# Optimization experiments

Measured on AMD Instinct MI355X. Metric: run time of the kernel, lower is better.

Reference implementation:

```python
import jax, jax.numpy as jnp
import numpy as np

Q = 9          # D2Q9
G = 8          # dihedral group of the square
X = YD = 768   # spatial grid
HID = 32       # tau_net hidden width
N_IN = 6       # moments with order <= 2 (indices 0..5, contiguous by construction)
LOWER_TAU = 0.8


def _build_stencil():
    # D2Q9 velocities and weights
    e = np.array([[0, 0], [1, 0], [0, 1], [-1, 0], [0, -1],
                  [1, 1], [-1, 1], [-1, -1], [1, -1]], dtype=np.float64)
    w = np.array([4 / 9] + [1 / 9] * 4 + [1 / 36] * 4, dtype=np.float64)
    # natural moment matrix: rows are monomials ex^px * ey^py, ordered so that
    # moment_order = [0,1,1,2,2,2,3,3,4]  ->  in_indices=[0..5], out_indices=[6,7,8]
    exps = [(0, 0), (1, 0), (0, 1), (2, 0), (1, 1), (0, 2), (2, 1), (1, 2), (2, 2)]
    M = np.stack([e[:, 0] ** px * e[:, 1] ** py for px, py in exps])  # [Q, Q]
    Minv = np.linalg.inv(M)
    # symmetry group of the square: 4 rotations x {id, x-axis reflection}
    rots = [np.array([[np.cos(a), -np.sin(a)], [np.sin(a), np.cos(a)]])
            for a in (0.0, np.pi / 2, np.pi, 3 * np.pi / 2)]
    refl = np.array([[1.0, 0.0], [0.0, -1.0]])
    Rs = rots + [r @ refl for r in rots]
    perms = []
    for R in Rs:
        Re = np.rint(e @ R.T)
        P = np.zeros((Q, Q))
        for i in range(Q):
            j = int(np.where((e == Re[i]).all(axis=1))[0][0])
            P[j, i] = 1.0  # velocity i maps to velocity j under R
        perms.append(P)
    P = np.stack(perms)                                   # [G, Q, Q]
    actions = np.einsum('qp,gpr,rs->gqs', M, P, Minv)      # moment action  M P M^-1
    Pt = P.transpose(0, 2, 1)                              # P^-1 = P^T
    inv_actions = np.einsum('qp,gpr,rs->gqs', M, Pt, Minv)
    return (M.astype(np.float32), Minv.astype(np.float32),
            actions.astype(np.float32), inv_actions.astype(np.float32),
            e.astype(np.float32), w.astype(np.float32))


def setup_inputs() -> dict:
    key = jax.random.key(0)
    kf, k1, k2, k3 = jax.random.split(key, 4)
    M, Minv, actions, inv_actions, e, w = _build_stencil()
    f = jax.random.uniform(kf, (Q, X, YD), dtype=jnp.float32)
    s = 0.1
    return {
        'f': f,
        'M': jnp.asarray(M), 'Minv': jnp.asarray(Minv),
        'actions': jnp.asarray(actions), 'inv_actions': jnp.asarray(inv_actions),
        'e': jnp.asarray(e), 'w': jnp.asarray(w),
        'W1': jax.random.normal(k1, (N_IN, HID), jnp.float32) * s,
        'b1': jnp.zeros((HID,), jnp.float32),
        'W2': jax.random.normal(k2, (HID, HID), jnp.float32) * s,
        'b2': jnp.zeros((HID,), jnp.float32),
        'W3': jax.random.normal(k3, (HID, Q - N_IN), jnp.float32) * s,
        'b3': jnp.zeros((Q - N_IN,), jnp.float32),
    }


def reference(f, M, Minv, actions, inv_actions, e, w, W1, b1, W2, b2, W3, b3):
    # --- moment transform: m = M f, moved to channel-last [X, Y, Q] ---
    m = jnp.einsum('qp,pxy->xyq', M, f)
    # --- equivariant tau net on low-order moments ---
    x_in = m[..., :N_IN]                                   # in_indices = 0..5
    Ainv = inv_actions[:, :N_IN, :N_IN]                    # [G, 6, 6]
    A = actions[:, N_IN:, N_IN:]                           # [G, 3, 3] (out_indices)
    xg = jnp.einsum('gij,xyj->gxyi', Ainv, x_in)           # [G, X, Y, 6]
    h = jax.nn.relu(xg @ W1 + b1)
    h = jax.nn.relu(h @ W2 + b2)
    o = h @ W3 + b3                                        # [G, X, Y, 3]
    out = jnp.einsum('gij,gxyj->xyi', A, o)                # sum over group -> [X, Y, 3]
    tau_hi = 1.5 + jax.nn.elu(out)                         # gt_half: > 0.5
    taus = jnp.full(m.shape, LOWER_TAU, m.dtype).at[..., N_IN:].set(tau_hi)
    # --- equilibrium moments: meq = M feq(rho, u) (quadratic BGK, cs^2=1/3) ---
    rho = m[..., 0:1]                                      # natural moments: m0=rho
    u = m[..., 1:3] / rho                                  # m1,m2 = momentum
    eu = jnp.einsum('qd,xyd->xyq', e, u)
    usq = jnp.sum(u * u, axis=-1, keepdims=True)
    feq = w * rho * (1.0 + 3.0 * eu + 4.5 * eu * eu - 1.5 * usq)
    meq = jnp.einsum('qp,xyp->xyq', M, feq)
    # --- MRT collision + inverse transform ---
    m_post = m - (m - meq) / taus
    return jnp.einsum('pq,xyq->pxy', Minv, m_post)
```

## Files before the change

kernel.cpp:

```cpp
#include <hip/hip_runtime.h>
#include <hip/hip_bf16.h>
#include <math.h>

#define Q 9
#define NPIX (768 * 768)

typedef short bf16x8 __attribute__((ext_vector_type(8)));
typedef short s16x2 __attribute__((ext_vector_type(2)));
typedef float f32x4 __attribute__((ext_vector_type(4)));
typedef float f32x16 __attribute__((ext_vector_type(16)));
typedef int i32x4 __attribute__((ext_vector_type(4)));

#define A3LOV 512
#define A3HIV 1024
#define A2LOV 1536
#define A2HIV 1600
#define B3TF  6656
#define WSHORTS 13312
#define WVEC4   (WSHORTS / 8)

__device__ __forceinline__ int hidmap(int k) {
    return (k & 3) + 8 * ((k >> 2) & 1) + 4 * (k >> 3);
}

__device__ __forceinline__ unsigned short f2bf(float x) {
    unsigned u = __builtin_bit_cast(unsigned, x);
    unsigned r = u + 0x7FFFu + ((u >> 16) & 1u);
    return (unsigned short)(r >> 16);
}

__device__ __forceinline__ unsigned pk2(float e, float o) {
    __hip_bfloat162 h = __float22bfloat162_rn(make_float2(e, o));
    unsigned u;
    __builtin_memcpy(&u, &h, 4);
    return u;
}

__device__ __forceinline__ unsigned relu2(unsigned d) {
    s16x2 v = __builtin_bit_cast(s16x2, d);
    const s16x2 z = {0, 0};
    v = __builtin_elementwise_max(v, z);
    return __builtin_bit_cast(unsigned, v);
}

__device__ __forceinline__ bf16x8 mk8(unsigned w0, unsigned w1, unsigned w2, unsigned w3) {
    i32x4 t = {(int)w0, (int)w1, (int)w2, (int)w3};
    return __builtin_bit_cast(bf16x8, t);
}

__global__ void prep_kernel(const float* __restrict__ actions,
                            const float* __restrict__ inv_actions,
                            const float* __restrict__ W1,
                            const float* __restrict__ b1,
                            const float* __restrict__ W2,
                            const float* __restrict__ W3,
                            const float* __restrict__ b3,
                            short* __restrict__ wsb,
                            float* __restrict__ wsf) {
    const int idx = blockIdx.x * 256 + threadIdx.x;
    if (idx < 4096) {
        int j = idx & 7, l = (idx >> 3) & 63, g = idx >> 9;
        int m = l & 31, k = (l >> 5) * 8 + j;
        float v = 0.f;
        if (k < 6) {
            #pragma unroll
            for (int i = 0; i < 6; i++)
                v += inv_actions[g * 81 + i * 9 + k] * W1[i * 32 + m];
        } else if (k == 6) v = b1[m];
        wsb[idx] = (short)f2bf(v);
    } else if (idx < 8192) {
        int t = idx - 4096;
        int j = t & 7, l = (t >> 3) & 63, g = t >> 9;
        int m = l & 31, kk = (l >> 5) * 8 + j, h = hidmap(kk);
        float v = 0.f;
        if (m < 3) {
            #pragma unroll
            for (int j3 = 0; j3 < 3; j3++)
                v += W3[h * 3 + j3] * actions[g * 81 + (6 + m) * 9 + (6 + j3)];
        }
        wsb[idx] = (short)f2bf(v);
    } else if (idx < 12288) {
        int t = idx - 8192;
        int j = t & 7, l = (t >> 3) & 63, g = t >> 9;
        int m = l & 31, kk = (l >> 5) * 8 + j, h = 16 + hidmap(kk);
        float v = 0.f;
        if (m < 3) {
            #pragma unroll
            for (int j3 = 0; j3 < 3; j3++)
                v += W3[h * 3 + j3] * actions[g * 81 + (6 + m) * 9 + (6 + j3)];
        }
        wsb[idx] = (short)f2bf(v);
    } else if (idx < 12800) {
        int t = idx - 12288;
        int j = t & 7, l = (t >> 3) & 63;
        int m = l & 31, kk = (l >> 5) * 8 + j;
        wsb[idx] = (short)f2bf(W2[hidmap(kk) * 32 + m]);
    } else if (idx < 13312) {
        int t = idx - 12800;
        int j = t & 7, l = (t >> 3) & 63;
        int m = l & 31, kk = (l >> 5) * 8 + j;
        wsb[idx] = (short)f2bf(W2[(16 + hidmap(kk)) * 32 + m]);
    } else if (idx < 13315) {
        int t = idx - 13312;
        float acc = 0.f;
        for (int g = 0; g < 8; g++)
            #pragma unroll
            for (int j = 0; j < 3; j++)
                acc += actions[g * 81 + (6 + t) * 9 + (6 + j)] * b3[j];
        wsf[B3TF + t] = acc;
    }
}

#define MLP_BODY(WA1, W3LO, W3HI, B1F, OACC)                                          \
    {                                                                                 \
        f32x16 C1 = __builtin_amdgcn_mfma_f32_32x32x16_bf16(WA1, B1F, z16, 0, 0, 0);  \
        bf16x8 B2lo = mk8(relu2(pk2(C1[0], C1[1])), relu2(pk2(C1[2], C1[3])),         \
                          relu2(pk2(C1[4], C1[5])), relu2(pk2(C1[6], C1[7])));        \
        bf16x8 B2hi = mk8(relu2(pk2(C1[8], C1[9])), relu2(pk2(C1[10], C1[11])),       \
                          relu2(pk2(C1[12], C1[13])), relu2(pk2(C1[14], C1[15])));    \
        f32x16 C2 = __builtin_amdgcn_mfma_f32_32x32x16_bf16(a2hi, B2hi, c2i, 0, 0, 0);\
        C2 = __builtin_amdgcn_mfma_f32_32x32x16_bf16(a2lo, B2lo, C2, 0, 0, 0);        \
        bf16x8 B3lo = mk8(relu2(pk2(C2[0], C2[1])), relu2(pk2(C2[2], C2[3])),         \
                          relu2(pk2(C2[4], C2[5])), relu2(pk2(C2[6], C2[7])));        \
        bf16x8 B3hi = mk8(relu2(pk2(C2[8], C2[9])), relu2(pk2(C2[10], C2[11])),       \
                          relu2(pk2(C2[12], C2[13])), relu2(pk2(C2[14], C2[15])));    \
        OACC = __builtin_amdgcn_mfma_f32_32x32x16_bf16(W3HI, B3hi, OACC, 0, 0, 0);    \
        OACC = __builtin_amdgcn_mfma_f32_32x32x16_bf16(W3LO, B3lo, OACC, 0, 0, 0);    \
    }

#define MOMENTS_PK(F0,F1,F2,F3,F4,F5,F6,F7,F8, MP0, MP1, MP2)                         \
    {                                                                                 \
        float sa = F5 + F6, sb = F7 + F8, sc = F5 - F6, sd = F7 - F8;                 \
        float sab = sa + sb;                                                          \
        float m4_ = sc + sd;                                                          \
        float p13 = F1 + F3, d13 = F1 - F3, p24 = F2 + F4, d24 = F2 - F4;             \
        float m0_ = F0 + p13 + p24 + sab;                                             \
        float m1_ = d13 + (sc - sd);                                                  \
        float m2_ = d24 + (sa - sb);                                                  \
        float m3_ = p13 + sab;                                                        \
        float m5_ = p24 + sab;                                                        \
        MP0 = pk2(m0_, m1_); MP1 = pk2(m2_, m3_); MP2 = pk2(m4_, m5_);                \
    }

__device__ __forceinline__ void epilogue(float fr0, float fr1, float fr2, float fr3,
                                         float fr4, float fr5, float fr6, float fr7,
                                         float fr8, f32x4 ov, int p,
                                         float* __restrict__ out) {
    float tinv[3];
    #pragma unroll
    for (int i = 0; i < 3; i++) {
        float o = ov[i];
        float el = (o > 0.f) ? o : (__expf(o) - 1.f);
        tinv[i] = __builtin_amdgcn_rcpf(1.5f + el);
    }
    float sa = fr5 + fr6, sb = fr7 + fr8, sc = fr5 - fr6, sd = fr7 - fr8;
    float p13 = fr1 + fr3, p24 = fr2 + fr4;
    float rho = fr0 + p13 + p24 + (sa + sb);
    float m1 = (fr1 - fr3) + (sc - sd);
    float m2 = (fr2 - fr4) + (sa - sb);

    float ir = __builtin_amdgcn_rcpf(rho);
    float ux = m1 * ir, uy = m2 * ir;
    float usq = ux * ux + uy * uy;
    float base = 1.f - 1.5f * usq;
    float w1r = rho * (1.f / 9.f), w5r = rho * (1.f / 36.f);
    float bx = 3.f * ux, ax = fmaf(4.5f * ux, ux, base);
    float feq1 = w1r * (ax + bx), feq3 = w1r * (ax - bx);
    float by = 3.f * uy, ay = fmaf(4.5f * uy, uy, base);
    float feq2 = w1r * (ay + by), feq4 = w1r * (ay - by);
    float ss = ux + uy, bs = 3.f * ss, as_ = fmaf(4.5f * ss, ss, base);
    float feq5 = w5r * (as_ + bs), feq7 = w5r * (as_ - bs);
    float dd = uy - ux, bd = 3.f * dd, ad = fmaf(4.5f * dd, dd, base);
    float feq6 = w5r * (ad + bd), feq8 = w5r * (ad - bd);

    float g1 = fr1 - feq1, g2 = fr2 - feq2, g3 = fr3 - feq3, g4 = fr4 - feq4;
    float g5 = fr5 - feq5, g6 = fr6 - feq6, g7 = fr7 - feq7, g8 = fr8 - feq8;
    float pa = g1 + g3, pb = g2 + g4;
    float ea = g5 + g6, eb = g7 + g8, ec = g5 - g6, ed = g7 - g8;
    float eab = ea + eb;
    float m3p = pa + eab, m5p = pb + eab, m8p = eab;
    float m6p = ea - eb, m4p = ec + ed, m7p = ec - ed;

    float d3 = 1.25f * m3p, h3 = 0.625f * m3p;
    float d5 = 1.25f * m5p, h5 = 0.625f * m5p;
    float k4 = 0.3125f * m4p;
    float h6 = (0.5f * tinv[0]) * m6p, k6 = 0.5f * h6;
    float h7 = (0.5f * tinv[1]) * m7p, k7 = 0.5f * h7;
    float d8 = tinv[2] * m8p, h8 = 0.5f * d8, k8 = 0.5f * h8;

    float c0 = d8 - d3 - d5;
    float c1 = h3 - h7 - h8;
    float c2 = h5 - h6 - h8;
    float c3 = h3 + h7 - h8;
    float c4 = h5 + h6 - h8;
    float sA = k4 + k7, sB = k6 + k8, sC = k4 + k8;
    float sD = k6 + k7, sE = k7 + k8, sF = k4 + k6;
    float c5 = sA + sB, c6 = sB - sA, c7 = sC - sD, c8 = sE - sF;

    __builtin_nontemporal_store(fr0 - c0, &out[0 * NPIX + p]);
    __builtin_nontemporal_store(fr1 - c1, &out[1 * NPIX + p]);
    __builtin_nontemporal_store(fr2 - c2, &out[2 * NPIX + p]);
    __builtin_nontemporal_store(fr3 - c3, &out[3 * NPIX + p]);
    __builtin_nontemporal_store(fr4 - c4, &out[4 * NPIX + p]);
    __builtin_nontemporal_store(fr5 - c5, &out[5 * NPIX + p]);
    __builtin_nontemporal_store(fr6 - c6, &out[6 * NPIX + p]);
    __builtin_nontemporal_store(fr7 - c7, &out[7 * NPIX + p]);
    __builtin_nontemporal_store(fr8 - c8, &out[8 * NPIX + p]);
}

__global__ __launch_bounds__(256, 3) void lbm_kernel(
    const float* __restrict__ f,
    const float* __restrict__ Minv,
    const float* __restrict__ w,
    const float* __restrict__ b2,
    const short* __restrict__ wsb,
    const float* __restrict__ wsf,
    float* __restrict__ out) {
    __shared__ float oL[4][64][4];
    __shared__ __align__(16) short wlds[WSHORTS];
    (void)Minv;
    (void)w;

    const int tid = threadIdx.x;
    const int wv = tid >> 6;
    const int l = tid & 63;
    const int hi = l >> 5;

    {
        const i32x4* src = (const i32x4*)wsb;
        i32x4* dst = (i32x4*)wlds;
        for (int i = tid; i < WVEC4; i += 256) dst[i] = src[i];
    }

    float b30 = wsf[B3TF + 0], b31 = wsf[B3TF + 1], b32 = wsf[B3TF + 2];
    f32x16 c2i;
    #pragma unroll
    for (int r = 0; r < 16; r++) {
        const int base = (r & 3) + 8 * (r >> 2);
        c2i[r] = hi ? b2[base + 4] : b2[base];
    }
    f32x16 oinit;
    #pragma unroll
    for (int r = 0; r < 16; r++) oinit[r] = 0.f;
    oinit[0] = hi ? 0.f : b30;
    oinit[1] = hi ? 0.f : b31;
    oinit[2] = hi ? 0.f : b32;
    f32x16 z16;
    #pragma unroll
    for (int r = 0; r < 16; r++) z16[r] = 0.f;

    __syncthreads();
    const bf16x8* wl = (const bf16x8*)wlds;
    bf16x8 a2lo = wl[A2LOV + l], a2hi = wl[A2HIV + l];

    const unsigned CONE = 0x00003F80u;
    const int s0 = (l & 31) << 2;
    const int s1 = s0 | (32 << 2);
    const int pbase = blockIdx.x * 768;

    #pragma unroll 1
    for (int t = 0; t < 3; t++) {
        const int p = pbase + t * 256 + tid;

        unsigned mp0, mp1, mp2;
        {
            float a0 = f[0 * NPIX + p], a1 = f[1 * NPIX + p], a2 = f[2 * NPIX + p];
            float a3 = f[3 * NPIX + p], a4 = f[4 * NPIX + p], a5 = f[5 * NPIX + p];
            float a6 = f[6 * NPIX + p], a7 = f[7 * NPIX + p], a8 = f[8 * NPIX + p];
            MOMENTS_PK(a0, a1, a2, a3, a4, a5, a6, a7, a8, mp0, mp1, mp2);
        }

        bf16x8 B1A = mk8((unsigned)__builtin_amdgcn_ds_bpermute(s0, (int)mp0),
                         (unsigned)__builtin_amdgcn_ds_bpermute(s0, (int)mp1),
                         (unsigned)__builtin_amdgcn_ds_bpermute(s0, (int)mp2), CONE);
        bf16x8 B1B = mk8((unsigned)__builtin_amdgcn_ds_bpermute(s1, (int)mp0),
                         (unsigned)__builtin_amdgcn_ds_bpermute(s1, (int)mp1),
                         (unsigned)__builtin_amdgcn_ds_bpermute(s1, (int)mp2), CONE);

        f32x16 oaccA = oinit, oaccB = oinit;

        bf16x8 wa1 = wl[l], w3lo = wl[A3LOV + l], w3hi = wl[A3HIV + l];
        #pragma unroll 1
        for (int g = 0; g < 7; g++) {
            const int gn = g + 1;
            bf16x8 na1  = wl[gn * 64 + l];
            bf16x8 n3lo = wl[A3LOV + gn * 64 + l];
            bf16x8 n3hi = wl[A3HIV + gn * 64 + l];
            MLP_BODY(wa1, w3lo, w3hi, B1A, oaccA);
            MLP_BODY(wa1, w3lo, w3hi, B1B, oaccB);
            wa1 = na1; w3lo = n3lo; w3hi = n3hi;
        }
        int p2 = p;
        asm("" : "+v"(p2));
        float r0 = f[0 * NPIX + p2], r1 = f[1 * NPIX + p2], r2 = f[2 * NPIX + p2];
        float r3 = f[3 * NPIX + p2], r4 = f[4 * NPIX + p2], r5 = f[5 * NPIX + p2];
        float r6 = f[6 * NPIX + p2], r7 = f[7 * NPIX + p2], r8 = f[8 * NPIX + p2];
        MLP_BODY(wa1, w3lo, w3hi, B1A, oaccA);
        MLP_BODY(wa1, w3lo, w3hi, B1B, oaccB);

        if (hi == 0) {
            const int lc = l & 31;
            f32x4 t0 = {oaccA[0], oaccA[1], oaccA[2], oaccA[3]};
            *(f32x4*)&oL[wv][lc][0] = t0;
            f32x4 t1 = {oaccB[0], oaccB[1], oaccB[2], oaccB[3]};
            *(f32x4*)&oL[wv][32 + lc][0] = t1;
        }
        f32x4 ov = *(const f32x4*)&oL[wv][l][0];

        epilogue(r0, r1, r2, r3, r4, r5, r6, r7, r8, ov, p, out);
    }
}

extern "C" void kernel_launch(void* const* d_in, const int* in_sizes, int n_in,
                              void* d_out, int out_size, void* d_ws, size_t ws_size,
                              hipStream_t stream) {
    const float* f           = (const float*)d_in[0];
    const float* Minv        = (const float*)d_in[2];
    const float* actions     = (const float*)d_in[3];
    const float* inv_actions = (const float*)d_in[4];
    const float* w           = (const float*)d_in[6];
    const float* W1          = (const float*)d_in[7];
    const float* b1          = (const float*)d_in[8];
    const float* W2          = (const float*)d_in[9];
    const float* b2          = (const float*)d_in[10];
    const float* W3          = (const float*)d_in[11];
    const float* b3          = (const float*)d_in[12];
    float* outp = (float*)d_out;
    short* wsb = (short*)d_ws;
    float* wsf = (float*)d_ws;

    prep_kernel<<<53, 256, 0, stream>>>(actions, inv_actions, W1, b1, W2, W3, b3, wsb, wsf);
    lbm_kernel<<<NPIX / 768, 256, 0, stream>>>(f, Minv, w, b2, wsb, wsf, outp);
}
```

Baseline: 121.1 us.

## Process one tile per block and shrink MLP output accumulators to scalars

Each block now handles 256 pixels instead of looping over three tiles, so the grid grows threefold and launch bounds rise to 4 blocks per CU. The layer-3 MFMA now accumulates into a fresh zeroed tile each group, and only three scalar values are summed into registers instead of keeping two 16-wide accumulators live. The b3 bias is added in the epilogue. This is meant to lower register pressure and raise occupancy, at the cost of reloading the weight table into LDS three times as often and issuing extra adds.

After: 121.2 us. About the same (+0.0%).

```diff
diff --git a/kernel.cpp b/kernel.cpp
--- a/kernel.cpp
+++ b/kernel.cpp
@@ -111,7 +111,7 @@
     }
 }
 
-#define MLP_BODY(WA1, W3LO, W3HI, B1F, OACC)                                          \
+#define MLP_BODY(WA1, W3LO, W3HI, B1F, A0, A1, A2)                                    \
     {                                                                                 \
         f32x16 C1 = __builtin_amdgcn_mfma_f32_32x32x16_bf16(WA1, B1F, z16, 0, 0, 0);  \
         bf16x8 B2lo = mk8(relu2(pk2(C1[0], C1[1])), relu2(pk2(C1[2], C1[3])),         \
@@ -124,8 +124,9 @@
                           relu2(pk2(C2[4], C2[5])), relu2(pk2(C2[6], C2[7])));        \
         bf16x8 B3hi = mk8(relu2(pk2(C2[8], C2[9])), relu2(pk2(C2[10], C2[11])),       \
                           relu2(pk2(C2[12], C2[13])), relu2(pk2(C2[14], C2[15])));    \
-        OACC = __builtin_amdgcn_mfma_f32_32x32x16_bf16(W3HI, B3hi, OACC, 0, 0, 0);    \
-        OACC = __builtin_amdgcn_mfma_f32_32x32x16_bf16(W3LO, B3lo, OACC, 0, 0, 0);    \
+        f32x16 C3 = __builtin_amdgcn_mfma_f32_32x32x16_bf16(W3HI, B3hi, z16, 0, 0, 0);\
+        C3 = __builtin_amdgcn_mfma_f32_32x32x16_bf16(W3LO, B3lo, C3, 0, 0, 0);        \
+        A0 += C3[0]; A1 += C3[1]; A2 += C3[2];                                        \
     }
 
 #define MOMENTS_PK(F0,F1,F2,F3,F4,F5,F6,F7,F8, MP0, MP1, MP2)                         \
@@ -142,22 +143,111 @@
         MP0 = pk2(m0_, m1_); MP1 = pk2(m2_, m3_); MP2 = pk2(m4_, m5_);                \
     }
 
-__device__ __forceinline__ void epilogue(float fr0, float fr1, float fr2, float fr3,
-                                         float fr4, float fr5, float fr6, float fr7,
-                                         float fr8, f32x4 ov, int p,
-                                         float* __restrict__ out) {
+__global__ __launch_bounds__(256, 4) void lbm_kernel(
+    const float* __restrict__ f,
+    const float* __restrict__ Minv,
+    const float* __restrict__ w,
+    const float* __restrict__ b2,
+    const short* __restrict__ wsb,
+    const float* __restrict__ wsf,
+    float* __restrict__ out) {
+    __shared__ float oL[4][64][4];
+    __shared__ __align__(16) short wlds[WSHORTS];
+    (void)Minv;
+    (void)w;
+
+    const int tid = threadIdx.x;
+    const int wv = tid >> 6;
+    const int l = tid & 63;
+    const int hi = l >> 5;
+    const int p = blockIdx.x * 256 + tid;
+
+    {
+        const i32x4* src = (const i32x4*)wsb;
+        i32x4* dst = (i32x4*)wlds;
+        for (int i = tid; i < WVEC4; i += 256) dst[i] = src[i];
+    }
+
+    unsigned mp0, mp1, mp2;
+    {
+        float a0 = f[0 * NPIX + p], a1 = f[1 * NPIX + p], a2 = f[2 * NPIX + p];
+        float a3 = f[3 * NPIX + p], a4 = f[4 * NPIX + p], a5 = f[5 * NPIX + p];
+        float a6 = f[6 * NPIX + p], a7 = f[7 * NPIX + p], a8 = f[8 * NPIX + p];
+        MOMENTS_PK(a0, a1, a2, a3, a4, a5, a6, a7, a8, mp0, mp1, mp2);
+    }
+
+    const unsigned CONE = 0x00003F80u;
+    const int s0 = (l & 31) << 2;
+    const int s1 = s0 | (32 << 2);
+    bf16x8 B1A = mk8((unsigned)__builtin_amdgcn_ds_bpermute(s0, (int)mp0),
+                     (unsigned)__builtin_amdgcn_ds_bpermute(s0, (int)mp1),
+                     (unsigned)__builtin_amdgcn_ds_bpermute(s0, (int)mp2), CONE);
+    bf16x8 B1B = mk8((unsigned)__builtin_amdgcn_ds_bpermute(s1, (int)mp0),
+                     (unsigned)__builtin_amdgcn_ds_bpermute(s1, (int)mp1),
+                     (unsigned)__builtin_amdgcn_ds_bpermute(s1, (int)mp2), CONE);
+
+    f32x16 c2i;
+    #pragma unroll
+    for (int r = 0; r < 16; r++) {
+        const int base = (r & 3) + 8 * (r >> 2);
+        c2i[r] = hi ? b2[base + 4] : b2[base];
+    }
+    f32x16 z16;
+    #pragma unroll
+    for (int r = 0; r < 16; r++) z16[r] = 0.f;
+    float accA0 = 0.f, accA1 = 0.f, accA2 = 0.f;
+    float accB0 = 0.f, accB1 = 0.f, accB2 = 0.f;
+
+    __syncthreads();
+    const bf16x8* wl = (const bf16x8*)wlds;
+    bf16x8 a2lo = wl[A2LOV + l], a2hi = wl[A2HIV + l];
+
+    bf16x8 wa1 = wl[l], w3lo = wl[A3LOV + l], w3hi = wl[A3HIV + l];
+    #pragma unroll 1
+    for (int g = 0; g < 7; g++) {
+        const int gn = g + 1;
+        bf16x8 na1  = wl[gn * 64 + l];
+        bf16x8 n3lo = wl[A3LOV + gn * 64 + l];
+        bf16x8 n3hi = wl[A3HIV + gn * 64 + l];
+        MLP_BODY(wa1, w3lo, w3hi, B1A, accA0, accA1, accA2);
+        MLP_BODY(wa1, w3lo, w3hi, B1B, accB0, accB1, accB2);
+        wa1 = na1; w3lo = n3lo; w3hi = n3hi;
+    }
+    int p2 = p;
+    asm("" : "+v"(p2));
+    float r0 = f[0 * NPIX + p2], r1 = f[1 * NPIX + p2], r2 = f[2 * NPIX + p2];
+    float r3 = f[3 * NPIX + p2], r4 = f[4 * NPIX + p2], r5 = f[5 * NPIX + p2];
+    float r6 = f[6 * NPIX + p2], r7 = f[7 * NPIX + p2], r8 = f[8 * NPIX + p2];
+    MLP_BODY(wa1, w3lo, w3hi, B1A, accA0, accA1, accA2);
+    MLP_BODY(wa1, w3lo, w3hi, B1B, accB0, accB1, accB2);
+
+    if (hi == 0) {
+        const int lc = l & 31;
+        f32x4 t0 = {accA0, accA1, accA2, 0.f};
+        *(f32x4*)&oL[wv][lc][0] = t0;
+        f32x4 t1 = {accB0, accB1, accB2, 0.f};
+        *(f32x4*)&oL[wv][32 + lc][0] = t1;
+    }
+    f32x4 ov = *(const f32x4*)&oL[wv][l][0];
+
+    float b3t0 = wsf[B3TF + 0], b3t1 = wsf[B3TF + 1], b3t2 = wsf[B3TF + 2];
+
     float tinv[3];
-    #pragma unroll
-    for (int i = 0; i < 3; i++) {
-        float o = ov[i];
-        float el = (o > 0.f) ? o : (__expf(o) - 1.f);
-        tinv[i] = __builtin_amdgcn_rcpf(1.5f + el);
-    }
-    float sa = fr5 + fr6, sb = fr7 + fr8, sc = fr5 - fr6, sd = fr7 - fr8;
-    float p13 = fr1 + fr3, p24 = fr2 + fr4;
-    float rho = fr0 + p13 + p24 + (sa + sb);
-    float m1 = (fr1 - fr3) + (sc - sd);
-    float m2 = (fr2 - fr4) + (sa - sb);
+    {
+        float o0 = ov[0] + b3t0, o1 = ov[1] + b3t1, o2 = ov[2] + b3t2;
+        float e0 = (o0 > 0.f) ? o0 : (__expf(o0) - 1.f);
+        float e1 = (o1 > 0.f) ? o1 : (__expf(o1) - 1.f);
+        float e2 = (o2 > 0.f) ? o2 : (__expf(o2) - 1.f);
+        tinv[0] = __builtin_amdgcn_rcpf(1.5f + e0);
+        tinv[1] = __builtin_amdgcn_rcpf(1.5f + e1);
+        tinv[2] = __builtin_amdgcn_rcpf(1.5f + e2);
+    }
+
+    float sa = r5 + r6, sb = r7 + r8, sc = r5 - r6, sd = r7 - r8;
+    float p13 = r1 + r3, p24 = r2 + r4;
+    float rho = r0 + p13 + p24 + (sa + sb);
+    float m1 = (r1 - r3) + (sc - sd);
+    float m2 = (r2 - r4) + (sa - sb);
 
     float ir = __builtin_amdgcn_rcpf(rho);
     float ux = m1 * ir, uy = m2 * ir;
@@ -173,8 +263,8 @@
     float dd = uy - ux, bd = 3.f * dd, ad = fmaf(4.5f * dd, dd, base);
     float feq6 = w5r * (ad + bd), feq8 = w5r * (ad - bd);
 
-    float g1 = fr1 - feq1, g2 = fr2 - feq2, g3 = fr3 - feq3, g4 = fr4 - feq4;
-    float g5 = fr5 - feq5, g6 = fr6 - feq6, g7 = fr7 - feq7, g8 = fr8 - feq8;
+    float g1 = r1 - feq1, g2 = r2 - feq2, g3 = r3 - feq3, g4 = r4 - feq4;
+    float g5 = r5 - feq5, g6 = r6 - feq6, g7 = r7 - feq7, g8 = r8 - feq8;
     float pa = g1 + g3, pb = g2 + g4;
     float ea = g5 + g6, eb = g7 + g8, ec = g5 - g6, ed = g7 - g8;
     float eab = ea + eb;
@@ -197,118 +287,15 @@
     float sD = k6 + k7, sE = k7 + k8, sF = k4 + k6;
     float c5 = sA + sB, c6 = sB - sA, c7 = sC - sD, c8 = sE - sF;
 
-    __builtin_nontemporal_store(fr0 - c0, &out[0 * NPIX + p]);
-    __builtin_nontemporal_store(fr1 - c1, &out[1 * NPIX + p]);
-    __builtin_nontemporal_store(fr2 - c2, &out[2 * NPIX + p]);
-    __builtin_nontemporal_store(fr3 - c3, &out[3 * NPIX + p]);
-    __builtin_nontemporal_store(fr4 - c4, &out[4 * NPIX + p]);
-    __builtin_nontemporal_store(fr5 - c5, &out[5 * NPIX + p]);
-    __builtin_nontemporal_store(fr6 - c6, &out[6 * NPIX + p]);
-    __builtin_nontemporal_store(fr7 - c7, &out[7 * NPIX + p]);
-    __builtin_nontemporal_store(fr8 - c8, &out[8 * NPIX + p]);
-}
-
-__global__ __launch_bounds__(256, 3) void lbm_kernel(
-    const float* __restrict__ f,
-    const float* __restrict__ Minv,
-    const float* __restrict__ w,
-    const float* __restrict__ b2,
-    const short* __restrict__ wsb,
-    const float* __restrict__ wsf,
-    float* __restrict__ out) {
-    __shared__ float oL[4][64][4];
-    __shared__ __align__(16) short wlds[WSHORTS];
-    (void)Minv;
-    (void)w;
-
-    const int tid = threadIdx.x;
-    const int wv = tid >> 6;
-    const int l = tid & 63;
-    const int hi = l >> 5;
-
-    {
-        const i32x4* src = (const i32x4*)wsb;
-        i32x4* dst = (i32x4*)wlds;
-        for (int i = tid; i < WVEC4; i += 256) dst[i] = src[i];
-    }
-
-    float b30 = wsf[B3TF + 0], b31 = wsf[B3TF + 1], b32 = wsf[B3TF + 2];
-    f32x16 c2i;
-    #pragma unroll
-    for (int r = 0; r < 16; r++) {
-        const int base = (r & 3) + 8 * (r >> 2);
-        c2i[r] = hi ? b2[base + 4] : b2[base];
-    }
-    f32x16 oinit;
-    #pragma unroll
-    for (int r = 0; r < 16; r++) oinit[r] = 0.f;
-    oinit[0] = hi ? 0.f : b30;
-    oinit[1] = hi ? 0.f : b31;
-    oinit[2] = hi ? 0.f : b32;
-    f32x16 z16;
-    #pragma unroll
-    for (int r = 0; r < 16; r++) z16[r] = 0.f;
-
-    __syncthreads();
-    const bf16x8* wl = (const bf16x8*)wlds;
-    bf16x8 a2lo = wl[A2LOV + l], a2hi = wl[A2HIV + l];
-
-    const unsigned CONE = 0x00003F80u;
-    const int s0 = (l & 31) << 2;
-    const int s1 = s0 | (32 << 2);
-    const int pbase = blockIdx.x * 768;
-
-    #pragma unroll 1
-    for (int t = 0; t < 3; t++) {
-        const int p = pbase + t * 256 + tid;
-
-        unsigned mp0, mp1, mp2;
-        {
-            float a0 = f[0 * NPIX + p], a1 = f[1 * NPIX + p], a2 = f[2 * NPIX + p];
-            float a3 = f[3 * NPIX + p], a4 = f[4 * NPIX + p], a5 = f[5 * NPIX + p];
-            float a6 = f[6 * NPIX + p], a7 = f[7 * NPIX + p], a8 = f[8 * NPIX + p];
-            MOMENTS_PK(a0, a1, a2, a3, a4, a5, a6, a7, a8, mp0, mp1, mp2);
-        }
-
-        bf16x8 B1A = mk8((unsigned)__builtin_amdgcn_ds_bpermute(s0, (int)mp0),
-                         (unsigned)__builtin_amdgcn_ds_bpermute(s0, (int)mp1),
-                         (unsigned)__builtin_amdgcn_ds_bpermute(s0, (int)mp2), CONE);
-        bf16x8 B1B = mk8((unsigned)__builtin_amdgcn_ds_bpermute(s1, (int)mp0),
-                         (unsigned)__builtin_amdgcn_ds_bpermute(s1, (int)mp1),
-                         (unsigned)__builtin_amdgcn_ds_bpermute(s1, (int)mp2), CONE);
-
-        f32x16 oaccA = oinit, oaccB = oinit;
-
-        bf16x8 wa1 = wl[l], w3lo = wl[A3LOV + l], w3hi = wl[A3HIV + l];
-        #pragma unroll 1
-        for (int g = 0; g < 7; g++) {
-            const int gn = g + 1;
-            bf16x8 na1  = wl[gn * 64 + l];
-            bf16x8 n3lo = wl[A3LOV + gn * 64 + l];
-            bf16x8 n3hi = wl[A3HIV + gn * 64 + l];
-            MLP_BODY(wa1, w3lo, w3hi, B1A, oaccA);
-            MLP_BODY(wa1, w3lo, w3hi, B1B, oaccB);
-            wa1 = na1; w3lo = n3lo; w3hi = n3hi;
-        }
-        int p2 = p;
-        asm("" : "+v"(p2));
-        float r0 = f[0 * NPIX + p2], r1 = f[1 * NPIX + p2], r2 = f[2 * NPIX + p2];
-        float r3 = f[3 * NPIX + p2], r4 = f[4 * NPIX + p2], r5 = f[5 * NPIX + p2];
-        float r6 = f[6 * NPIX + p2], r7 = f[7 * NPIX + p2], r8 = f[8 * NPIX + p2];
-        MLP_BODY(wa1, w3lo, w3hi, B1A, oaccA);
-        MLP_BODY(wa1, w3lo, w3hi, B1B, oaccB);
-
-        if (hi == 0) {
-            const int lc = l & 31;
-            f32x4 t0 = {oaccA[0], oaccA[1], oaccA[2], oaccA[3]};
-            *(f32x4*)&oL[wv][lc][0] = t0;
-            f32x4 t1 = {oaccB[0], oaccB[1], oaccB[2], oaccB[3]};
-            *(f32x4*)&oL[wv][32 + lc][0] = t1;
-        }
-        f32x4 ov = *(const f32x4*)&oL[wv][l][0];
-
-        epilogue(r0, r1, r2, r3, r4, r5, r6, r7, r8, ov, p, out);
-    }
+    __builtin_nontemporal_store(r0 - c0, &out[0 * NPIX + p]);
+    __builtin_nontemporal_store(r1 - c1, &out[1 * NPIX + p]);
+    __builtin_nontemporal_store(r2 - c2, &out[2 * NPIX + p]);
+    __builtin_nontemporal_store(r3 - c3, &out[3 * NPIX + p]);
+    __builtin_nontemporal_store(r4 - c4, &out[4 * NPIX + p]);
+    __builtin_nontemporal_store(r5 - c5, &out[5 * NPIX + p]);
+    __builtin_nontemporal_store(r6 - c6, &out[6 * NPIX + p]);
+    __builtin_nontemporal_store(r7 - c7, &out[7 * NPIX + p]);
+    __builtin_nontemporal_store(r8 - c8, &out[8 * NPIX + p]);
 }
 
 extern "C" void kernel_launch(void* const* d_in, const int* in_sizes, int n_in,
@@ -330,5 +317,5 @@
     float* wsf = (float*)d_ws;
 
     prep_kernel<<<53, 256, 0, stream>>>(actions, inv_actions, W1, b1, W2, W3, b3, wsb, wsf);
-    lbm_kernel<<<NPIX / 768, 256, 0, stream>>>(f, Minv, w, b2, wsb, wsf, outp);
-}
+    lbm_kernel<<<NPIX / 256, 256, 0, stream>>>(f, Minv, w, b2, wsb, wsf, outp);
+}
```
